# Optimization experiments

Hardware: AMD Instinct MI355X
Metric: run time of the kernel (lower is better)

Reference implementation:

```python
import jax, jax.numpy as jnp
import numpy as np

KERNEL_SIZE = 5


def setup_inputs() -> dict:
    key = jax.random.key(0)
    k1, k2, k3 = jax.random.split(key, 3)
    B, H, W = 32, 512, 512
    f = jax.random.uniform(k1, (B, H, W), dtype=jnp.float32)          # distribution function, non-negative
    K = jax.random.normal(k2, (KERNEL_SIZE, KERNEL_SIZE, H, W), dtype=jnp.float32) * 0.01  # per-pixel kernels
    dt = jax.random.uniform(k3, (B,), dtype=jnp.float32) * 0.1        # per-batch timestep
    return {"f": f, "K": K, "dt": dt}


def reference(f, K, dt):
    # f: (B,H,W); K: (k,k,H,W) position-dependent (unshared) kernels; dt: (B,)
    # Equivalent to: patches = unfold(pad(f)); df = einsum('bkv,kv->bv', patches, K.reshape(k*k,-1))
    # Implemented as a sum over the k*k kernel taps of shifted slices (avoids the
    # B*k^2*H*W patches tensor; loop is over the fixed kernel footprint, not data dims).
    k = K.shape[0]
    B, H, W = f.shape
    pl, pr = k // 2, (k - 1) // 2  # matches pad_size = (k//2, (k-1)//2)*2
    f_pad = jnp.pad(f, ((0, 0), (pl, pr), (pl, pr)))  # 'zeros' padding_mode
    df = jnp.zeros_like(f)
    for i in range(k):
        for j in range(k):
            df = df + f_pad[:, i:i + H, j:j + W] * K[i, j]
    out = f + df * dt[:, None, None]
    return jnp.maximum(out, 0.0)  # ensure_non_negative_f clamp
```

## Files before the change

### kernel.cpp

```cpp
#include <hip/hip_runtime.h>

#define H 512
#define W 512
#define HW (H * W)
#define BATCH 32
#define KS 5
#define NBH 8
#define NSTEP (NBH * KS)
#define PD 3

typedef float nf4 __attribute__((ext_vector_type(4)));

__global__ __launch_bounds__(128, 2) void op2d_kernel(
    const float* __restrict__ f,
    const float* __restrict__ K,
    const float* __restrict__ dt,
    float* __restrict__ out)
{
    const int tid = threadIdx.x;
    const int w0  = tid * 4;
    const int bx  = blockIdx.x;
    const int r   = (bx & 7) * 64 + (bx >> 3);
    const int b0  = blockIdx.y * NBH;

    const bool wl = (w0 >= 4);
    const bool wr = (w0 <= 504);

    int rowoff[KS];
    bool inb[KS];
#pragma unroll
    for (int i = 0; i < KS; ++i) {
        const int gr = r + i - 2;
        inb[i] = (gr >= 0) && (gr < H);
        rowoff[i] = (gr < 0 ? 0 : (gr >= H ? H - 1 : gr)) * W;
    }

    nf4 rbuf[PD][3];
#define ISSUE(s, d)                                                          \
    {                                                                        \
        const float* fb = f + (size_t)(b0 + (s) / KS) * HW                   \
                            + rowoff[(s) % KS] + w0;                         \
        (d)[0] = wl ? *reinterpret_cast<const nf4*>(fb - 4) : (nf4)0.f;      \
        (d)[1] =      *reinterpret_cast<const nf4*>(fb);                     \
        (d)[2] = wr ? *reinterpret_cast<const nf4*>(fb + 4) : (nf4)0.f;      \
    }

#pragma unroll
    for (int s = 0; s < PD; ++s) ISSUE(s, rbuf[s]);

    nf4 Kt[KS * KS];
#pragma unroll
    for (int i = 0; i < KS; ++i) {
        if (inb[i]) {
#pragma unroll
            for (int j = 0; j < KS; ++j)
                Kt[i * KS + j] = *reinterpret_cast<const nf4*>(
                    K + ((size_t)(i * KS + j) * H + r) * W + w0);
        } else {
#pragma unroll
            for (int j = 0; j < KS; ++j) Kt[i * KS + j] = (nf4)0.f;
        }
    }

    float dtb[NBH];
#pragma unroll
    for (int bi = 0; bi < NBH; ++bi) dtb[bi] = dt[b0 + bi];

    float acc[4] = {0.f, 0.f, 0.f, 0.f};
    float fc[4]  = {0.f, 0.f, 0.f, 0.f};

#pragma unroll
    for (int s = 0; s < NSTEP; ++s) {
        const int bi = s / KS;
        const int i  = s % KS;

        const nf4 ra = rbuf[s % PD][0];
        const nf4 rb = rbuf[s % PD][1];
        const nf4 rc = rbuf[s % PD][2];
        if (s + PD < NSTEP) ISSUE(s + PD, rbuf[(s + PD) % PD]);

        const float buf[12] = { ra.x, ra.y, ra.z, ra.w,
                                rb.x, rb.y, rb.z, rb.w,
                                rc.x, rc.y, rc.z, rc.w };
        if (i == 2) { fc[0] = rb.x; fc[1] = rb.y; fc[2] = rb.z; fc[3] = rb.w; }

#pragma unroll
        for (int j = 0; j < KS; ++j) {
            const nf4 kv = Kt[i * KS + j];
            acc[0] += kv.x * buf[j + 2];
            acc[1] += kv.y * buf[j + 3];
            acc[2] += kv.z * buf[j + 4];
            acc[3] += kv.w * buf[j + 5];
        }

        if (i == KS - 1) {
            nf4 o;
            o.x = fmaxf(fc[0] + acc[0] * dtb[bi], 0.f);
            o.y = fmaxf(fc[1] + acc[1] * dtb[bi], 0.f);
            o.z = fmaxf(fc[2] + acc[2] * dtb[bi], 0.f);
            o.w = fmaxf(fc[3] + acc[3] * dtb[bi], 0.f);
            __builtin_nontemporal_store(o, reinterpret_cast<nf4*>(
                out + ((size_t)(b0 + bi) * H + r) * W + w0));
            acc[0] = acc[1] = acc[2] = acc[3] = 0.f;
        }
    }
#undef ISSUE
}

extern "C" void kernel_launch(void* const* d_in, const int* in_sizes, int n_in,
                              void* d_out, int out_size, void* d_ws, size_t ws_size,
                              hipStream_t stream) {
    const float* f  = (const float*)d_in[0];
    const float* K  = (const float*)d_in[1];
    const float* dt = (const float*)d_in[2];
    float* out = (float*)d_out;

    dim3 block(128);
    dim3 grid(H, BATCH / NBH);
    op2d_kernel<<<grid, block, 0, stream>>>(f, K, dt, out);
}
```

Baseline: 131.0 us.

## Reorder loop to kernel-row outer, batch inner, streaming K rows

Swaps loop order so each kernel row of K is loaded once and applied to all batches, keeping only two rows of K in registers (double-buffered) instead of all 25 taps. Halves batches per block to 4 and raises the launch-bounds occupancy hint to 3 blocks per CU, doubling the grid. The centre value f is now reloaded separately for the epilogue rather than captured during accumulation. K is read twice as often overall since each block covers fewer batches, and the extra f reloads add traffic.

```diff
diff --git a/kernel.cpp b/kernel.cpp
--- a/kernel.cpp
+++ b/kernel.cpp
@@ -5,13 +5,13 @@
 #define HW (H * W)
 #define BATCH 32
 #define KS 5
-#define NBH 8
-#define NSTEP (NBH * KS)
+#define NBH 4
+#define NSTEP (KS * NBH)
 #define PD 3
 
 typedef float nf4 __attribute__((ext_vector_type(4)));
 
-__global__ __launch_bounds__(128, 2) void op2d_kernel(
+__global__ __launch_bounds__(128, 3) void op2d_kernel(
     const float* __restrict__ f,
     const float* __restrict__ K,
     const float* __restrict__ dt,
@@ -36,75 +36,85 @@
     }
 
     nf4 rbuf[PD][3];
-#define ISSUE(s, d)                                                          \
+#define FISSUE(s)                                                            \
     {                                                                        \
-        const float* fb = f + (size_t)(b0 + (s) / KS) * HW                   \
-                            + rowoff[(s) % KS] + w0;                         \
-        (d)[0] = wl ? *reinterpret_cast<const nf4*>(fb - 4) : (nf4)0.f;      \
-        (d)[1] =      *reinterpret_cast<const nf4*>(fb);                     \
-        (d)[2] = wr ? *reinterpret_cast<const nf4*>(fb + 4) : (nf4)0.f;      \
+        const float* fb = f + (size_t)(b0 + (s) % NBH) * HW                  \
+                            + rowoff[(s) / NBH] + w0;                        \
+        rbuf[(s) % PD][0] = wl ? *(const nf4*)(fb - 4) : (nf4)0.f;           \
+        rbuf[(s) % PD][1] =      *(const nf4*)(fb);                          \
+        rbuf[(s) % PD][2] = wr ? *(const nf4*)(fb + 4) : (nf4)0.f;           \
     }
 
 #pragma unroll
-    for (int s = 0; s < PD; ++s) ISSUE(s, rbuf[s]);
+    for (int s = 0; s < PD; ++s) FISSUE(s);
 
-    nf4 Kt[KS * KS];
+    nf4 Kb[2][KS];
 #pragma unroll
-    for (int i = 0; i < KS; ++i) {
-        if (inb[i]) {
-#pragma unroll
-            for (int j = 0; j < KS; ++j)
-                Kt[i * KS + j] = *reinterpret_cast<const nf4*>(
-                    K + ((size_t)(i * KS + j) * H + r) * W + w0);
-        } else {
-#pragma unroll
-            for (int j = 0; j < KS; ++j) Kt[i * KS + j] = (nf4)0.f;
-        }
-    }
+    for (int j = 0; j < KS; ++j)
+        Kb[0][j] = inb[0] ? *(const nf4*)(K + ((size_t)j * H + r) * W + w0)
+                          : (nf4)0.f;
 
     float dtb[NBH];
 #pragma unroll
     for (int bi = 0; bi < NBH; ++bi) dtb[bi] = dt[b0 + bi];
 
-    float acc[4] = {0.f, 0.f, 0.f, 0.f};
-    float fc[4]  = {0.f, 0.f, 0.f, 0.f};
+    float acc[NBH][4] = {};
+    nf4 fcr[2];
 
 #pragma unroll
-    for (int s = 0; s < NSTEP; ++s) {
-        const int bi = s / KS;
-        const int i  = s % KS;
+    for (int i = 0; i < KS; ++i) {
+#pragma unroll
+        for (int bi = 0; bi < NBH; ++bi) {
+            const int s = i * NBH + bi;
 
-        const nf4 ra = rbuf[s % PD][0];
-        const nf4 rb = rbuf[s % PD][1];
-        const nf4 rc = rbuf[s % PD][2];
-        if (s + PD < NSTEP) ISSUE(s + PD, rbuf[(s + PD) % PD]);
+            const nf4 ra = rbuf[s % PD][0];
+            const nf4 rb = rbuf[s % PD][1];
+            const nf4 rc = rbuf[s % PD][2];
+            if (s + PD < NSTEP) FISSUE(s + PD);
 
-        const float buf[12] = { ra.x, ra.y, ra.z, ra.w,
-                                rb.x, rb.y, rb.z, rb.w,
-                                rc.x, rc.y, rc.z, rc.w };
-        if (i == 2) { fc[0] = rb.x; fc[1] = rb.y; fc[2] = rb.z; fc[3] = rb.w; }
+            if (bi == 0 && i + 1 < KS) {
+#pragma unroll
+                for (int j = 0; j < KS; ++j)
+                    Kb[(i + 1) & 1][j] = inb[i + 1]
+                        ? *(const nf4*)(K + ((size_t)((i + 1) * KS + j) * H + r) * W + w0)
+                        : (nf4)0.f;
+            }
+
+            if (i == KS - 2 && bi >= NBH - 2) {
+                const int bt = bi - (NBH - 2);
+                fcr[bt & 1] = *(const nf4*)(f + (size_t)(b0 + bt) * HW
+                                              + (size_t)r * W + w0);
+            }
+
+            const float buf[12] = { ra.x, ra.y, ra.z, ra.w,
+                                    rb.x, rb.y, rb.z, rb.w,
+                                    rc.x, rc.y, rc.z, rc.w };
 
 #pragma unroll
-        for (int j = 0; j < KS; ++j) {
-            const nf4 kv = Kt[i * KS + j];
-            acc[0] += kv.x * buf[j + 2];
-            acc[1] += kv.y * buf[j + 3];
-            acc[2] += kv.z * buf[j + 4];
-            acc[3] += kv.w * buf[j + 5];
-        }
+            for (int j = 0; j < KS; ++j) {
+                const nf4 kv = Kb[i & 1][j];
+                acc[bi][0] += kv.x * buf[j + 2];
+                acc[bi][1] += kv.y * buf[j + 3];
+                acc[bi][2] += kv.z * buf[j + 4];
+                acc[bi][3] += kv.w * buf[j + 5];
+            }
 
-        if (i == KS - 1) {
-            nf4 o;
-            o.x = fmaxf(fc[0] + acc[0] * dtb[bi], 0.f);
-            o.y = fmaxf(fc[1] + acc[1] * dtb[bi], 0.f);
-            o.z = fmaxf(fc[2] + acc[2] * dtb[bi], 0.f);
-            o.w = fmaxf(fc[3] + acc[3] * dtb[bi], 0.f);
-            __builtin_nontemporal_store(o, reinterpret_cast<nf4*>(
-                out + ((size_t)(b0 + bi) * H + r) * W + w0));
-            acc[0] = acc[1] = acc[2] = acc[3] = 0.f;
+            if (i == KS - 1) {
+                const nf4 fc = fcr[bi & 1];
+                if (bi + 2 < NBH)
+                    fcr[bi & 1] = *(const nf4*)(f + (size_t)(b0 + bi + 2) * HW
+                                                  + (size_t)r * W + w0);
+                nf4 o;
+                o.x = fmaxf(fc.x + acc[bi][0] * dtb[bi], 0.f);
+                o.y = fmaxf(fc.y + acc[bi][1] * dtb[bi], 0.f);
+                o.z = fmaxf(fc.z + acc[bi][2] * dtb[bi], 0.f);
+                o.w = fmaxf(fc.w + acc[bi][3] * dtb[bi], 0.f);
+                __builtin_nontemporal_store(o,
+                    (nf4*)(out + ((size_t)(b0 + bi) * H + r) * W + w0));
+            }
         }
     }
-#undef ISSUE
+#undef FISSUE
 }
 
 extern "C" void kernel_launch(void* const* d_in, const int* in_sizes, int n_in,
```

New measurement: 330.6 us. 152% more time.

## Switch to 2-wide columns with 256 threads and whole-batch double-buffered row prefetch

Applied to the files above, without the earlier changes.

Each thread now handles 2 columns instead of 4, so a 256-thread block covers the 512-wide row. The per-row 3-deep load pipeline becomes a double buffer holding all 5 rows of the next batch, and the swizzled row ordering is dropped. The aim is to put more threads and more loads in flight per block to better hide memory latency. The cost is narrower 8-byte loads, a loss of L2 locality from removing the row swizzle, and more register pressure from holding two 5-row windows.

```diff
diff --git a/kernel.cpp b/kernel.cpp
--- a/kernel.cpp
+++ b/kernel.cpp
@@ -6,28 +6,24 @@
 #define BATCH 32
 #define KS 5
 #define NBH 8
-#define NSTEP (NBH * KS)
-#define PD 3
 
-typedef float nf4 __attribute__((ext_vector_type(4)));
+typedef float nf2 __attribute__((ext_vector_type(2)));
 
-__global__ __launch_bounds__(128, 2) void op2d_kernel(
+__global__ __launch_bounds__(256, 1) void op2d_kernel(
     const float* __restrict__ f,
     const float* __restrict__ K,
     const float* __restrict__ dt,
     float* __restrict__ out)
 {
     const int tid = threadIdx.x;
-    const int w0  = tid * 4;
-    const int bx  = blockIdx.x;
-    const int r   = (bx & 7) * 64 + (bx >> 3);
+    const int c0  = tid * 2;
+    const int r   = blockIdx.x;
     const int b0  = blockIdx.y * NBH;
 
-    const bool wl = (w0 >= 4);
-    const bool wr = (w0 <= 504);
+    const bool wl = (c0 >= 2);
+    const bool wr = (c0 <= 508);
 
-    int rowoff[KS];
-    bool inb[KS];
+    int rowoff[KS]; bool inb[KS];
 #pragma unroll
     for (int i = 0; i < KS; ++i) {
         const int gr = r + i - 2;
@@ -35,76 +31,59 @@
         rowoff[i] = (gr < 0 ? 0 : (gr >= H ? H - 1 : gr)) * W;
     }
 
-    nf4 rbuf[PD][3];
-#define ISSUE(s, d)                                                          \
-    {                                                                        \
-        const float* fb = f + (size_t)(b0 + (s) / KS) * HW                   \
-                            + rowoff[(s) % KS] + w0;                         \
-        (d)[0] = wl ? *reinterpret_cast<const nf4*>(fb - 4) : (nf4)0.f;      \
-        (d)[1] =      *reinterpret_cast<const nf4*>(fb);                     \
-        (d)[2] = wr ? *reinterpret_cast<const nf4*>(fb + 4) : (nf4)0.f;      \
+    nf2 win[2][KS][3];
+#define FROW(b, i, d) {                                                      \
+        const float* fp = f + (size_t)(b0 + (b)) * HW + rowoff[i] + c0;      \
+        (d)[0] = wl ? *(const nf2*)(fp - 2) : (nf2)0.f;                      \
+        (d)[1] =      *(const nf2*)(fp);                                     \
+        (d)[2] = wr ? *(const nf2*)(fp + 2) : (nf2)0.f;                      \
     }
 
 #pragma unroll
-    for (int s = 0; s < PD; ++s) ISSUE(s, rbuf[s]);
+    for (int i = 0; i < KS; ++i) FROW(0, i, win[0][i]);
 
-    nf4 Kt[KS * KS];
+    nf2 Kt[KS][KS];
 #pragma unroll
     for (int i = 0; i < KS; ++i) {
-        if (inb[i]) {
 #pragma unroll
-            for (int j = 0; j < KS; ++j)
-                Kt[i * KS + j] = *reinterpret_cast<const nf4*>(
-                    K + ((size_t)(i * KS + j) * H + r) * W + w0);
-        } else {
-#pragma unroll
-            for (int j = 0; j < KS; ++j) Kt[i * KS + j] = (nf4)0.f;
-        }
+        for (int j = 0; j < KS; ++j)
+            Kt[i][j] = inb[i]
+                ? *(const nf2*)(K + (size_t)(i * KS + j) * HW
+                                  + (size_t)r * W + c0)
+                : (nf2)0.f;
     }
 
-    float dtb[NBH];
 #pragma unroll
-    for (int bi = 0; bi < NBH; ++bi) dtb[bi] = dt[b0 + bi];
-
-    float acc[4] = {0.f, 0.f, 0.f, 0.f};
-    float fc[4]  = {0.f, 0.f, 0.f, 0.f};
-
+    for (int b = 0; b < NBH; ++b) {
+        if (b + 1 < NBH) {
 #pragma unroll
-    for (int s = 0; s < NSTEP; ++s) {
-        const int bi = s / KS;
-        const int i  = s % KS;
-
-        const nf4 ra = rbuf[s % PD][0];
-        const nf4 rb = rbuf[s % PD][1];
-        const nf4 rc = rbuf[s % PD][2];
-        if (s + PD < NSTEP) ISSUE(s + PD, rbuf[(s + PD) % PD]);
-
-        const float buf[12] = { ra.x, ra.y, ra.z, ra.w,
-                                rb.x, rb.y, rb.z, rb.w,
-                                rc.x, rc.y, rc.z, rc.w };
-        if (i == 2) { fc[0] = rb.x; fc[1] = rb.y; fc[2] = rb.z; fc[3] = rb.w; }
-
-#pragma unroll
-        for (int j = 0; j < KS; ++j) {
-            const nf4 kv = Kt[i * KS + j];
-            acc[0] += kv.x * buf[j + 2];
-            acc[1] += kv.y * buf[j + 3];
-            acc[2] += kv.z * buf[j + 4];
-            acc[3] += kv.w * buf[j + 5];
+            for (int i = 0; i < KS; ++i) FROW(b + 1, i, win[(b + 1) & 1][i]);
         }
 
-        if (i == KS - 1) {
-            nf4 o;
-            o.x = fmaxf(fc[0] + acc[0] * dtb[bi], 0.f);
-            o.y = fmaxf(fc[1] + acc[1] * dtb[bi], 0.f);
-            o.z = fmaxf(fc[2] + acc[2] * dtb[bi], 0.f);
-            o.w = fmaxf(fc[3] + acc[3] * dtb[bi], 0.f);
-            __builtin_nontemporal_store(o, reinterpret_cast<nf4*>(
-                out + ((size_t)(b0 + bi) * H + r) * W + w0));
-            acc[0] = acc[1] = acc[2] = acc[3] = 0.f;
+        const float dtv = dt[b0 + b];
+
+        float ax = 0.f, ay = 0.f;
+#pragma unroll
+        for (int i = 0; i < KS; ++i) {
+            const nf2 e0 = win[b & 1][i][0];
+            const nf2 e1 = win[b & 1][i][1];
+            const nf2 e2 = win[b & 1][i][2];
+            const float w[6] = { e0.x, e0.y, e1.x, e1.y, e2.x, e2.y };
+#pragma unroll
+            for (int j = 0; j < KS; ++j) {
+                ax += Kt[i][j].x * w[j];
+                ay += Kt[i][j].y * w[j + 1];
+            }
         }
+
+        const nf2 fc = win[b & 1][2][1];
+        nf2 o;
+        o.x = fmaxf(fc.x + ax * dtv, 0.f);
+        o.y = fmaxf(fc.y + ay * dtv, 0.f);
+        __builtin_nontemporal_store(o,
+            (nf2*)(out + ((size_t)(b0 + b) * H + r) * W + c0));
     }
-#undef ISSUE
+#undef FROW
 }
 
 extern "C" void kernel_launch(void* const* d_in, const int* in_sizes, int n_in,
@@ -115,7 +94,7 @@
     const float* dt = (const float*)d_in[2];
     float* out = (float*)d_out;
 
-    dim3 block(128);
+    dim3 block(256);
     dim3 grid(H, BATCH / NBH);
     op2d_kernel<<<grid, block, 0, stream>>>(f, K, dt, out);
 }
```

Result: slower. 137.3 us (+4.8%).
